# Kernel tuning notes

Measured on AMD Instinct MI355X. Metric: run time of the kernel, lower is better.

## Reference

```python
import jax, jax.numpy as jnp
import numpy as np

B, T, S, D, H, F = 4, 1024, 1024, 1024, 16, 4096
NEG = jnp.float32(-1e9)


def _ln(x, g, b):
    m = jnp.mean(x, axis=-1, keepdims=True)
    v = jnp.mean((x - m) ** 2, axis=-1, keepdims=True)
    return (x - m) * jax.lax.rsqrt(v + 1e-5) * g + b


def _mha(q, k, v, wq, bq, wk, bk, wv, bv, wo, bo, scale, mask, causal, sbias):
    Bq, Tq, Dq = q.shape
    Sk = k.shape[1]
    dk = Dq // H
    Q = (q @ wq.T + bq).reshape(Bq, Tq, H, dk).transpose(0, 2, 1, 3)  # [B,H,T,dk]
    K = (k @ wk.T + bk).reshape(Bq, Sk, H, dk).transpose(0, 2, 1, 3)  # [B,H,S,dk]
    V = (v @ wv.T + bv).reshape(Bq, Sk, H, dk).transpose(0, 2, 1, 3)
    s = jnp.einsum('bhtd,bhsd->bhts', Q, K) / jnp.sqrt(jnp.float32(dk))
    if sbias is not None:
        s = s + scale * sbias[:, None, None, :]
    if mask is not None:
        s = jnp.where(mask == 0, NEG, s)
    if causal is not None:
        s = jnp.where(causal == 0, NEG, s)
    a = jax.nn.softmax(s, axis=-1)
    o = jnp.einsum('bhts,bhsd->bhtd', a, V).transpose(0, 2, 1, 3).reshape(Bq, Tq, Dq)
    return o @ wo.T + bo


def setup_inputs():
    key = jax.random.key(0)
    ks = jax.random.split(key, 16)
    r = lambda i, shape, s=0.02: jax.random.normal(ks[i], shape, dtype=jnp.float32) * s
    z = lambda *shape: jnp.zeros(shape, jnp.float32)
    o = lambda *shape: jnp.ones(shape, jnp.float32)
    inp = dict(
        x=r(0, (B, T, D), 1.0),
        memory=r(1, (B, S, D), 1.0),
        sentence_bias=r(2, (B, S), 1.0),
        trg_mask=jnp.ones((B, 1, 1, T), jnp.int32),
        trg_causal_mask=jnp.tril(jnp.ones((T, T), jnp.int32))[None, None],
        src_mask=jnp.ones((B, 1, 1, S), jnp.int32),
        sa_wq=r(3, (D, D)), sa_bq=z(D), sa_wk=r(4, (D, D)), sa_bk=z(D),
        sa_wv=r(5, (D, D)), sa_bv=z(D), sa_wo=r(6, (D, D)), sa_bo=z(D),
        sa_scale=jnp.float32(0.1),
        ca_wq=r(7, (D, D)), ca_bq=z(D), ca_wk=r(8, (D, D)), ca_bk=z(D),
        ca_wv=r(9, (D, D)), ca_bv=z(D), ca_wo=r(10, (D, D)), ca_bo=z(D),
        ca_scale=jnp.float32(0.1),
        ln1_g=o(D), ln1_b=z(D), ln2_g=o(D), ln2_b=z(D), ln3_g=o(D), ln3_b=z(D),
        ffn_w1=r(11, (F, D)), ffn_b1=z(F), ffn_w2=r(12, (D, F)), ffn_b2=z(D),
    )
    return inp


def reference(x, memory, trg_mask, trg_causal_mask, src_mask, sentence_bias,
              sa_wq, sa_bq, sa_wk, sa_bk, sa_wv, sa_bv, sa_wo, sa_bo, sa_scale,
              ca_wq, ca_bq, ca_wk, ca_bk, ca_wv, ca_bv, ca_wo, ca_bo, ca_scale,
              ln1_g, ln1_b, ln2_g, ln2_b, ln3_g, ln3_b,
              ffn_w1, ffn_b1, ffn_w2, ffn_b2):
    # Faithful quirk: Q comes from normed x, K/V from raw residual stream.
    x = x + _mha(_ln(x, ln1_g, ln1_b), x, x,
                 sa_wq, sa_bq, sa_wk, sa_bk, sa_wv, sa_bv, sa_wo, sa_bo,
                 sa_scale, trg_mask, trg_causal_mask, None)
    x = x + _mha(_ln(x, ln2_g, ln2_b), memory, memory,
                 ca_wq, ca_bq, ca_wk, ca_bk, ca_wv, ca_bv, ca_wo, ca_bo,
                 ca_scale, src_mask, None, sentence_bias)
    h = _ln(x, ln3_g, ln3_b)
    x = x + (jax.nn.relu(h @ ffn_w1.T + ffn_b1) @ ffn_w2.T + ffn_b2)
    return x
```

## Files before the change

### kernel.cpp

```cpp
#include <hip/hip_runtime.h>
#include <hip/hip_bf16.h>
#include <cmath>
#include <stdint.h>

typedef __hip_bfloat16 bf16;
typedef __attribute__((ext_vector_type(8))) __bf16 bf16x8;
typedef __attribute__((ext_vector_type(8))) unsigned short u16x8;
typedef __attribute__((ext_vector_type(4))) float f32x4;

__device__ __forceinline__ void gld16(const void* g, const void* l)
{
    __builtin_amdgcn_global_load_lds(
        (const __attribute__((address_space(1))) unsigned int*)(unsigned long long)g,
        (__attribute__((address_space(3))) unsigned int*)(unsigned int)(unsigned long long)l,
        16, 0, 0);
}

struct CvtSrcs { const float* p[24]; };

__global__ __launch_bounds__(256) void cvt_all(
    CvtSrcs s, bf16* __restrict__ dst,
    const float* __restrict__ lg, const float* __restrict__ lb,
    bf16* __restrict__ lnout)
{
    const int t = threadIdx.x;
    const int i = (blockIdx.x * 256 + t) * 8;
    const int seg = i >> 20;
    const float* sp = s.p[seg] + (i & 1048575);
    const float4 a = *(const float4*)(sp);
    const float4 b = *(const float4*)(sp + 4);
    const float v[8] = {a.x, a.y, a.z, a.w, b.x, b.y, b.z, b.w};
    bf16 tmp[8];
#pragma unroll
    for (int j = 0; j < 8; ++j) tmp[j] = __float2bfloat16(v[j]);
    *(uint4*)(dst + i) = *(const uint4*)tmp;

    if (seg < 4) {
        float s1 = 0.f, s2 = 0.f;
#pragma unroll
        for (int j = 0; j < 8; ++j) { s1 += v[j]; s2 += v[j] * v[j]; }
#pragma unroll
        for (int off = 32; off > 0; off >>= 1) {
            s1 += __shfl_xor(s1, off, 64);
            s2 += __shfl_xor(s2, off, 64);
        }
        __shared__ float r1[4], r2[4];
        const int w = t >> 6;
        if ((t & 63) == 0) { r1[w] = s1; r2[w] = s2; }
        __syncthreads();
        const int rw = (w >> 1) * 2;
        s1 = r1[rw] + r1[rw + 1];
        s2 = r2[rw] + r2[rw + 1];
        const float mean = s1 * (1.f / 1024.f);
        const float var  = s2 * (1.f / 1024.f) - mean * mean;
        const float rstd = rsqrtf(var + 1e-5f);
        bf16 lt[8];
        const int c0 = i & 1023;
#pragma unroll
        for (int j = 0; j < 8; ++j)
            lt[j] = __float2bfloat16((v[j] - mean) * rstd * lg[c0 + j] + lb[c0 + j]);
        *(uint4*)(lnout + i) = *(const uint4*)lt;
    }
}

enum {
    EPI_QSCALE = 0,
    EPI_KV = 1,
    EPI_RELU = 2,
    EPI_RES_F32_F32OUT = 3,
    EPI_PART = 4
};

template <int EPI>
__global__ __launch_bounds__(512, 2) void gemm256(
    const bf16* __restrict__ A, const bf16* __restrict__ W,
    const float* __restrict__ bias, void* __restrict__ out,
    int N, int Kiter, int Kstride)
{
    __shared__ __align__(16) unsigned short sA[2][2][128 * 64];
    __shared__ __align__(16) unsigned short sB[2][2][128 * 64];

    const int t  = threadIdx.x;
    const int l  = t & 63;
    const int w  = t >> 6;
    const int wv = w * 64;
    const int wr = w >> 2;
    const int wc = w & 3;
    const int lm = l & 15;
    const int kq = l >> 4;
    const int rx = lm & 7;

    int bx = blockIdx.x;
    const int xcd = bx & 7;
    const int ib  = bx >> 3;
    const int bm  = xcd * 2 + (ib & 1);
    const int bn  = ib >> 1;

    const bf16* gA = A + (size_t)(bm * 256 + (t >> 3)) * Kstride
                       + ((t & 7) ^ ((t >> 3) & 7)) * 8;
    const bf16* gB = W + (size_t)(bn * 256 + (t >> 3)) * Kstride
                       + ((t & 7) ^ ((t >> 3) & 7)) * 8;

#define SQA(slot, kt, j)                                        \
    gld16(gA + (size_t)((j) * 64) * Kstride + (kt) * 64,        \
          &sA[slot][(j) >> 1][(((j) & 1) * 512 + wv) * 8])
#define SQB(slot, kt, j)                                        \
    gld16(gB + (size_t)((j) * 64) * Kstride + (kt) * 64,        \
          &sB[slot][(j) >> 1][(((j) & 1) * 512 + wv) * 8])

    bf16x8 af[4][2], bg[2][2];

#define READ_AF(s_, mh)                                                     \
    do {                                                                    \
        _Pragma("unroll")                                                   \
        for (int mi = 0; mi < 4; ++mi)                                      \
            _Pragma("unroll")                                               \
            for (int kk = 0; kk < 2; ++kk) {                                \
                const int lr = (mh) * 64 + mi * 16 + lm;                    \
                const int sl = ((kk << 2) | kq) ^ rx;                       \
                af[mi][kk] = __builtin_bit_cast(bf16x8,                     \
                    *(const u16x8*)(&sA[s_][wr][lr * 64 + sl * 8]));        \
            }                                                               \
    } while (0)
#define READ_BG(s_, nh)                                                     \
    do {                                                                    \
        _Pragma("unroll")                                                   \
        for (int ni = 0; ni < 2; ++ni)                                      \
            _Pragma("unroll")                                               \
            for (int kk = 0; kk < 2; ++kk) {                                \
                const int lr = (wc & 1) * 64 + (nh) * 32 + ni * 16 + lm;    \
                const int sl = ((kk << 2) | kq) ^ rx;                       \
                bg[ni][kk] = __builtin_bit_cast(bf16x8,                     \
                    *(const u16x8*)(&sB[s_][wc >> 1][lr * 64 + sl * 8]));   \
            }                                                               \
    } while (0)
#define MFMA_QUAD(mh, nh)                                                   \
    do {                                                                    \
        __builtin_amdgcn_s_setprio(1);                                      \
        _Pragma("unroll")                                                   \
        for (int mi = 0; mi < 4; ++mi)                                      \
            _Pragma("unroll")                                               \
            for (int ni = 0; ni < 2; ++ni)                                  \
                _Pragma("unroll")                                           \
                for (int kk = 0; kk < 2; ++kk)                              \
                    acc[(mh) * 4 + mi][(nh) * 2 + ni] =                     \
                        __builtin_amdgcn_mfma_f32_16x16x32_bf16(            \
                            af[mi][kk], bg[ni][kk],                         \
                            acc[(mh) * 4 + mi][(nh) * 2 + ni], 0, 0, 0);    \
        __builtin_amdgcn_s_setprio(0);                                      \
    } while (0)
#define BARRIER() do { __builtin_amdgcn_s_barrier();                        \
                       __builtin_amdgcn_sched_barrier(0); } while (0)
#define WAITV4() asm volatile("s_waitcnt vmcnt(4)" ::: "memory")
#define WAITV2() asm volatile("s_waitcnt vmcnt(2)" ::: "memory")
#define WAITV0() asm volatile("s_waitcnt vmcnt(0)" ::: "memory")

    f32x4 acc[8][4] = {};
    const int NT = Kiter >> 6;

    SQB(0, 0, 0); SQB(0, 0, 1); SQB(0, 0, 2); SQB(0, 0, 3);
    SQA(0, 0, 0); SQA(0, 0, 2); SQA(0, 0, 1); SQA(0, 0, 3);

    for (int tt = 0; tt < NT - 1; ++tt) {
        const int s = tt & 1, d = s ^ 1, kn = tt + 1;
        WAITV2(); BARRIER();
        SQB(d, kn, 0); SQB(d, kn, 1);
        READ_AF(s, 0); READ_BG(s, 0);
        MFMA_QUAD(0, 0);
        WAITV2(); BARRIER();
        SQB(d, kn, 2); SQB(d, kn, 3);
        READ_AF(s, 1);
        MFMA_QUAD(1, 0);
        SQA(d, kn, 0); SQA(d, kn, 2);
        READ_BG(s, 1);
        MFMA_QUAD(1, 1);
        SQA(d, kn, 1); SQA(d, kn, 3);
        READ_AF(s, 0);
        MFMA_QUAD(0, 1);
    }
    {
        const int s = (NT - 1) & 1;
        WAITV2(); BARRIER();
        READ_AF(s, 0); READ_BG(s, 0);
        MFMA_QUAD(0, 0);
        WAITV0(); BARRIER();
        READ_AF(s, 1);
        MFMA_QUAD(1, 0);
        READ_BG(s, 1);
        MFMA_QUAD(1, 1);
        READ_AF(s, 0);
        MFMA_QUAD(0, 1);
    }

    __syncthreads();
    unsigned short* scr = (w < 4) ? &sA[0][0][0] + w * 8192
                                  : &sB[0][0][0] + (w - 4) * 8192;

#pragma unroll
    for (int NI = 0; NI < 4; ++NI) {
        const int col = bn * 256 + wc * 64 + NI * 16 + lm;
        const float bv = bias[col];
        const int c  = NI * 2 + (lm >> 3);
        const int ci = lm & 7;
#pragma unroll
        for (int MI = 0; MI < 8; ++MI) {
#pragma unroll
            for (int r = 0; r < 4; ++r) {
                float v = acc[MI][NI][r] + bv;
                if (EPI == EPI_RELU) v = fmaxf(v, 0.f);
                const int row = MI * 16 + kq * 4 + r;
                scr[row * 64 + ((c ^ (row & 7)) * 8) + ci] =
                    __builtin_bit_cast(unsigned short, (__bf16)v);
            }
        }
    }
#pragma unroll
    for (int it = 0; it < 16; ++it) {
        const int row = it * 8 + (l >> 3);
        const int lc  = l & 7;
        const u16x8 vv = *(const u16x8*)&scr[row * 64 + ((lc ^ (row & 7)) * 8)];
        const int Crow = bm * 256 + wr * 128 + row;
        const int Ccol = bn * 256 + wc * 64 + lc * 8;
        *(u16x8*)((bf16*)out + (size_t)Crow * N + Ccol) = vv;
    }
#undef SQA
#undef SQB
#undef READ_AF
#undef READ_BG
#undef MFMA_QUAD
}

template <int EPI>
__global__ __launch_bounds__(256, 2) void gemm_bt(
    const bf16* __restrict__ A, const bf16* __restrict__ W,
    const float* __restrict__ bias, const float* __restrict__ bias2,
    const float* __restrict__ res, void* __restrict__ out,
    int M, int N, int Kiter, int Kstride)
{
    __shared__ __align__(16) unsigned short sA[2][128 * 64];
    __shared__ __align__(16) unsigned short sB[2][128 * 64];

    const int t  = threadIdx.x;
    const int l  = t & 63;
    const int w  = t >> 6;
    const int wv = w * 64;
    const int wm = (w >> 1) * 64;
    const int wn = (w & 1) * 64;
    const int lm = l & 15;
    const int kq = l >> 4;
    const int rx = lm & 7;

    const int bx  = blockIdx.x;
    const int xcd = bx & 7;
    const int ib  = bx >> 3;
    const int bm  = xcd * 4 + (ib & 3);
    const int bn  = ib >> 2;

    const bf16* gA = A + (size_t)(bm * 128 + (t >> 3)) * Kstride
                       + ((t & 7) ^ ((t >> 3) & 7)) * 8;
    const bf16* gB = W + (size_t)(bn * 128 + (t >> 3)) * Kstride
                       + ((t & 7) ^ ((t >> 3) & 7)) * 8;

#define SQA(slot, kt, j)                                        \
    gld16(gA + (size_t)((j) * 32) * Kstride + (kt) * 64,        \
          &sA[slot][((j) * 256 + wv) * 8])
#define SQB(slot, kt, j)                                        \
    gld16(gB + (size_t)((j) * 32) * Kstride + (kt) * 64,        \
          &sB[slot][((j) * 256 + wv) * 8])

    bf16x8 af[2][2], bg[2][2];

#define READ_AF(s_, mh)                                                     \
    do {                                                                    \
        _Pragma("unroll")                                                   \
        for (int mi = 0; mi < 2; ++mi)                                      \
            _Pragma("unroll")                                               \
            for (int kk = 0; kk < 2; ++kk) {                                \
                const int lr = wm + (mh) * 32 + mi * 16 + lm;               \
                const int sl = ((kk << 2) | kq) ^ rx;                       \
                af[mi][kk] = __builtin_bit_cast(bf16x8,                     \
                    *(const u16x8*)(&sA[s_][lr * 64 + sl * 8]));            \
            }                                                               \
    } while (0)
#define READ_BG(s_, nh)                                                     \
    do {                                                                    \
        _Pragma("unroll")                                                   \
        for (int ni = 0; ni < 2; ++ni)                                      \
            _Pragma("unroll")                                               \
            for (int kk = 0; kk < 2; ++kk) {                                \
                const int lr = wn + (nh) * 32 + ni * 16 + lm;               \
                const int sl = ((kk << 2) | kq) ^ rx;                       \
                bg[ni][kk] = __builtin_bit_cast(bf16x8,                     \
                    *(const u16x8*)(&sB[s_][lr * 64 + sl * 8]));            \
            }                                                               \
    } while (0)
#define MFMA_QUAD(mh, nh)                                                   \
    do {                                                                    \
        __builtin_amdgcn_s_setprio(1);                                      \
        _Pragma("unroll")                                                   \
        for (int mi = 0; mi < 2; ++mi)                                      \
            _Pragma("unroll")                                               \
            for (int ni = 0; ni < 2; ++ni)                                  \
                _Pragma("unroll")                                           \
                for (int kk = 0; kk < 2; ++kk)                              \
                    acc[(mh) * 2 + mi][(nh) * 2 + ni] =                     \
                        __builtin_amdgcn_mfma_f32_16x16x32_bf16(            \
                            af[mi][kk], bg[ni][kk],                         \
                            acc[(mh) * 2 + mi][(nh) * 2 + ni], 0, 0, 0);    \
        __builtin_amdgcn_s_setprio(0);                                      \
    } while (0)

    f32x4 acc[4][4] = {};
    const int NT = Kiter >> 6;

    SQB(0, 0, 0); SQB(0, 0, 2); SQA(0, 0, 0); SQA(0, 0, 2);
    SQB(0, 0, 1); SQB(0, 0, 3); SQA(0, 0, 1); SQA(0, 0, 3);

    for (int tt = 0; tt < NT - 1; ++tt) {
        const int s = tt & 1, d = s ^ 1, kn = tt + 1;
        WAITV4(); BARRIER();
        SQB(d, kn, 0); SQB(d, kn, 2);
        READ_AF(s, 0); READ_BG(s, 0);
        MFMA_QUAD(0, 0);
        WAITV2(); BARRIER();
        SQA(d, kn, 0); SQA(d, kn, 2);
        READ_AF(s, 1);
        MFMA_QUAD(1, 0);
        SQB(d, kn, 1); SQB(d, kn, 3);
        READ_BG(s, 1);
        MFMA_QUAD(1, 1);
        SQA(d, kn, 1); SQA(d, kn, 3);
        READ_AF(s, 0);
        MFMA_QUAD(0, 1);
    }
    {
        const int s = (NT - 1) & 1;
        WAITV4(); BARRIER();
        READ_AF(s, 0); READ_BG(s, 0);
        MFMA_QUAD(0, 0);
        WAITV0(); BARRIER();
        READ_AF(s, 1);
        MFMA_QUAD(1, 0);
        READ_BG(s, 1);
        MFMA_QUAD(1, 1);
        READ_AF(s, 0);
        MFMA_QUAD(0, 1);
    }
#undef SQA
#undef SQB
#undef READ_AF
#undef READ_BG
#undef MFMA_QUAD
#undef BARRIER
#undef WAITV4
#undef WAITV2
#undef WAITV0

#pragma unroll
    for (int ni = 0; ni < 4; ++ni) {
        const int col = bn * 128 + wn + ni * 16 + lm;
        float bv = 0.f;
        if (EPI == EPI_KV) bv = (col < 1024) ? bias[col] : bias2[col - 1024];
        else bv = bias[col];
#pragma unroll
        for (int mi = 0; mi < 4; ++mi) {
#pragma unroll
            for (int r = 0; r < 4; ++r) {
                const int row = bm * 128 + wm + mi * 16 + kq * 4 + r;
                float v = acc[mi][ni][r] + bv;
                if (EPI == EPI_QSCALE) v *= 0.125f;
                if (EPI == EPI_KV) {
                    if (col < 1024) {
                        ((bf16*)out)[(size_t)row * 1024 + col] = __float2bfloat16(v);
                    } else {
                        const int ch = col - 1024;
                        const size_t idx = (size_t)4 * 1048576 +
                            ((size_t)((row >> 10) * 16 + (ch >> 6)) * 64 + (ch & 63)) * 1024
                            + (row & 1023);
                        ((bf16*)out)[idx] = __float2bfloat16(v);
                    }
                } else if (EPI == EPI_RES_F32_F32OUT) {
                    const size_t idx = (size_t)row * N + col;
                    ((float*)out)[idx] = v + res[idx];
                } else {
                    ((bf16*)out)[(size_t)row * N + col] = __float2bfloat16(v);
                }
            }
        }
    }
}

template <bool CAUSAL, bool SBIAS>
__global__ __launch_bounds__(256, 2) void flash_attn(
    const bf16* __restrict__ Q, const bf16* __restrict__ K,
    const bf16* __restrict__ Vt, bf16* __restrict__ O,
    const float* __restrict__ sbias, const float* __restrict__ scale_ptr)
{
    __shared__ __align__(16) unsigned short sK[2][64 * 64];
    __shared__ __align__(16) unsigned short sV[2][64 * 64];
    __shared__ __align__(16) unsigned short sP[4 * 32 * 72];

    const int t  = threadIdx.x;
    const int l  = t & 63;
    const int w  = t >> 6;
    const int wv = w * 64;
    const int lm = l & 15;
    const int kq = l >> 4;

    const int bh = blockIdx.x & 63;
    const int qb = blockIdx.x >> 6;
    const int h  = bh & 15;
    const int b  = bh >> 4;

    const int tb = qb * 128 + w * 32;
    const size_t qrow0 = (size_t)(b * 1024 + tb) * 1024 + h * 64;

    bf16x8 qf[2][2];
#pragma unroll
    for (int mi = 0; mi < 2; ++mi)
#pragma unroll
        for (int kk = 0; kk < 2; ++kk)
            qf[mi][kk] = __builtin_bit_cast(bf16x8,
                *(const u16x8*)(Q + qrow0 + (size_t)(mi * 16 + lm) * 1024 + kk * 32 + kq * 8));

    float cs = 0.f; const float* sb = nullptr;
    if (SBIAS) { cs = scale_ptr[0]; sb = sbias + b * 1024; }

    const bf16* gK = K  + (size_t)(b * 1024 + (t >> 3)) * 1024 + h * 64
                   + ((t & 7) ^ ((t >> 3) & 7)) * 8;
    const bf16* gV = Vt + (size_t)((b * 16 + h) * 64 + (t >> 3)) * 1024
                   + ((t & 7) ^ ((t >> 3) & 7)) * 8;
    __bf16* sPw = (__bf16*)sP + w * 32 * 72;

#define STAGE_KV(buf, s0r)                                                   \
    do {                                                                     \
        gld16(gK + (size_t)(s0r) * 1024,        &sK[buf][wv * 8]);           \
        gld16(gK + (size_t)((s0r) + 32) * 1024, &sK[buf][2048 + wv * 8]);    \
        gld16(gV + (s0r),                       &sV[buf][wv * 8]);           \
        gld16(gV + (s0r) + 32 * 1024,           &sV[buf][2048 + wv * 8]);    \
    } while (0)

    const int niter = CAUSAL ? (2 * qb + 2) : 16;

    STAGE_KV(0, 0);
    __syncthreads();

    f32x4 acc_o[2][4] = {};
    f32x4 l_run[2] = {};

    for (int it = 0; it < niter; ++it) {
        const int s0 = it * 64;
        const int cur = it & 1;

        if (it + 1 < niter) STAGE_KV(cur ^ 1, s0 + 64);

        f32x4 accs[2][4] = {};
#pragma unroll
        for (int ni = 0; ni < 4; ++ni)
#pragma unroll
            for (int kk = 0; kk < 2; ++kk) {
                const bf16x8 kf = __builtin_bit_cast(bf16x8,
                    *(const u16x8*)(&sK[cur][(ni * 16 + lm) * 64
                        + ((((kk << 2) | kq)) ^ (lm & 7)) * 8]));
#pragma unroll
                for (int mi = 0; mi < 2; ++mi)
                    accs[mi][ni] = __builtin_amdgcn_mfma_f32_16x16x32_bf16(
                        qf[mi][kk], kf, accs[mi][ni], 0, 0, 0);
            }

        if (SBIAS) {
#pragma unroll
            for (int ni = 0; ni < 4; ++ni) {
                const float sv = cs * sb[s0 + ni * 16 + lm];
#pragma unroll
                for (int mi = 0; mi < 2; ++mi)
#pragma unroll
                    for (int r = 0; r < 4; ++r) accs[mi][ni][r] += sv;
            }
        }
        if (CAUSAL && (s0 + 63 > tb)) {
#pragma unroll
            for (int ni = 0; ni < 4; ++ni) {
                const int s = s0 + ni * 16 + lm;
#pragma unroll
                for (int mi = 0; mi < 2; ++mi)
#pragma unroll
                    for (int r = 0; r < 4; ++r)
                        if (s > tb + mi * 16 + kq * 4 + r) accs[mi][ni][r] = -1e30f;
            }
        }

#pragma unroll
        for (int mi = 0; mi < 2; ++mi)
#pragma unroll
            for (int ni = 0; ni < 4; ++ni)
#pragma unroll
                for (int r = 0; r < 4; ++r) {
                    const float e = __expf(accs[mi][ni][r]);
                    l_run[mi][r] += e;
                    sPw[(mi * 16 + kq * 4 + r) * 72 + ni * 16 + lm] = (__bf16)e;
                }

#pragma unroll
        for (int kk = 0; kk < 2; ++kk) {
            bf16x8 pf[2];
#pragma unroll
            for (int mi = 0; mi < 2; ++mi)
                pf[mi] = __builtin_bit_cast(bf16x8,
                    *(const u16x8*)(sPw + (mi * 16 + lm) * 72 + kk * 32 + kq * 8));
#pragma unroll
            for (int di = 0; di < 4; ++di) {
                const bf16x8 vf = __builtin_bit_cast(bf16x8,
                    *(const u16x8*)(&sV[cur][(di * 16 + lm) * 64
                        + ((((kk << 2) | kq)) ^ (lm & 7)) * 8]));
#pragma unroll
                for (int mi = 0; mi < 2; ++mi)
                    acc_o[mi][di] = __builtin_amdgcn_mfma_f32_16x16x32_bf16(
                        pf[mi], vf, acc_o[mi][di], 0, 0, 0);
            }
        }

        __syncthreads();
    }
#undef STAGE_KV

#pragma unroll
    for (int mi = 0; mi < 2; ++mi) {
        f32x4 lt = l_run[mi];
#pragma unroll
        for (int x = 1; x < 16; x <<= 1)
#pragma unroll
            for (int r = 0; r < 4; ++r) lt[r] += __shfl_xor(lt[r], x, 64);
#pragma unroll
        for (int r = 0; r < 4; ++r) lt[r] = 1.f / lt[r];
#pragma unroll
        for (int di = 0; di < 4; ++di)
#pragma unroll
            for (int r = 0; r < 4; ++r) {
                const size_t idx = (size_t)(b * 1024 + tb + mi * 16 + kq * 4 + r) * 1024
                                 + h * 64 + di * 16 + lm;
                O[idx] = __float2bfloat16(acc_o[mi][di][r] * lt[r]);
            }
    }
}

__global__ __launch_bounds__(256) void ln_kernel(
    const float* __restrict__ xin, const float* __restrict__ g,
    const float* __restrict__ bta, bf16* __restrict__ out)
{
    const int row = blockIdx.x;
    const int t = threadIdx.x;
    const size_t base = (size_t)row * 1024 + t * 4;

    const float4 f = *(const float4*)(xin + base);
    const float v[4] = {f.x, f.y, f.z, f.w};
    float s1 = v[0] + v[1] + v[2] + v[3];
    float s2 = v[0]*v[0] + v[1]*v[1] + v[2]*v[2] + v[3]*v[3];
#pragma unroll
    for (int off = 32; off > 0; off >>= 1) {
        s1 += __shfl_xor(s1, off, 64);
        s2 += __shfl_xor(s2, off, 64);
    }
    __shared__ float r1[4], r2[4];
    if ((t & 63) == 0) { r1[t >> 6] = s1; r2[t >> 6] = s2; }
    __syncthreads();
    s1 = r1[0] + r1[1] + r1[2] + r1[3];
    s2 = r2[0] + r2[1] + r2[2] + r2[3];
    const float mean = s1 * (1.f / 1024.f);
    const float var  = s2 * (1.f / 1024.f) - mean * mean;
    const float rstd = rsqrtf(var + 1e-5f);
#pragma unroll
    for (int j = 0; j < 4; ++j) {
        const int c = t * 4 + j;
        out[base + j] = __float2bfloat16((v[j] - mean) * rstd * g[c] + bta[c]);
    }
}

extern "C" void kernel_launch(void* const* d_in, const int* in_sizes, int n_in,
                              void* d_out, int out_size, void* d_ws, size_t ws_size,
                              hipStream_t stream)
{
    const float* x       = (const float*)d_in[0];
    const float* memory  = (const float*)d_in[1];
    const float* sbias   = (const float*)d_in[2];
    const float* sa_bq = (const float*)d_in[7];
    const float* sa_bk = (const float*)d_in[9];
    const float* sa_bv = (const float*)d_in[11];
    const float* sa_bo = (const float*)d_in[13];
    const float* ca_bq = (const float*)d_in[16];
    const float* ca_bk = (const float*)d_in[18];
    const float* ca_bv = (const float*)d_in[20];
    const float* ca_bo = (const float*)d_in[22];
    const float* ca_scale = (const float*)d_in[23];
    const float* ln1_g = (const float*)d_in[24]; const float* ln1_b = (const float*)d_in[25];
    const float* ln2_g = (const float*)d_in[26]; const float* ln2_b = (const float*)d_in[27];
    const float* ln3_g = (const float*)d_in[28]; const float* ln3_b = (const float*)d_in[29];
    const float* b1 = (const float*)d_in[31];
    const float* b2 = (const float*)d_in[33];

    char* ws = (char*)d_ws;
    const size_t MB = (size_t)1 << 20;
    float* x1    = (float*)(ws + 0 * MB);
    float* x2    = (float*)(ws + 16 * MB);
    bf16* lnbuf  = (bf16*)(ws + 32 * MB);
    bf16* Qb     = (bf16*)(ws + 40 * MB);
    bf16* Kb     = (bf16*)(ws + 48 * MB);
    bf16* Vtb    = (bf16*)(ws + 56 * MB);
    bf16* Ob     = (bf16*)(ws + 64 * MB);
    bf16* ffnmid = (bf16*)(ws + 40 * MB);
    bf16* wx     = (bf16*)(ws + 72 * MB);
    bf16* wmem   = (bf16*)(ws + 80 * MB);
    bf16* bw     = (bf16*)(ws + 88 * MB);
    bf16* b_sa_wq = bw + 0 * 1048576, *b_sa_wk = bw + 1 * 1048576;
    bf16* b_sa_wo = bw + 3 * 1048576;
    bf16* b_ca_wq = bw + 4 * 1048576, *b_ca_wk = bw + 5 * 1048576;
    bf16* b_ca_wo = bw + 7 * 1048576;
    bf16* b_w1   = (bf16*)(ws + 104 * MB);
    bf16* b_w2   = (bf16*)(ws + 112 * MB);

    const int M = 4096;
    dim3 blk256(256), blk512(512);
    const dim3 gQ(256);
    const dim3 gKV(512);
    const dim3 gFA(512);
    const dim3 g256(256);

    CvtSrcs cs;
    for (int c = 0; c < 4; ++c) {
        cs.p[c]      = x + (size_t)c * 1048576;
        cs.p[4 + c]  = memory + (size_t)c * 1048576;
        cs.p[16 + c] = (const float*)d_in[30] + (size_t)c * 1048576;
        cs.p[20 + c] = (const float*)d_in[32] + (size_t)c * 1048576;
    }
    cs.p[8]  = (const float*)d_in[6];
    cs.p[9]  = (const float*)d_in[8];
    cs.p[10] = (const float*)d_in[10];
    cs.p[11] = (const float*)d_in[12];
    cs.p[12] = (const float*)d_in[15];
    cs.p[13] = (const float*)d_in[17];
    cs.p[14] = (const float*)d_in[19];
    cs.p[15] = (const float*)d_in[21];
    cvt_all<<<24 * 1048576 / 2048, blk256, 0, stream>>>(
        cs, wx, ln1_g, ln1_b, lnbuf);

    gemm_bt<EPI_QSCALE><<<gQ, blk256, 0, stream>>>(
        lnbuf, b_sa_wq, sa_bq, nullptr, nullptr, Qb, M, 1024, 1024, 1024);
    gemm_bt<EPI_KV><<<gKV, blk256, 0, stream>>>(
        wx, b_sa_wk, sa_bk, sa_bv, nullptr, Kb, M, 2048, 1024, 1024);
    flash_attn<true, false><<<gFA, blk256, 0, stream>>>(Qb, Kb, Vtb, Ob, nullptr, nullptr);
    gemm_bt<EPI_RES_F32_F32OUT><<<gQ, blk256, 0, stream>>>(
        Ob, b_sa_wo, sa_bo, nullptr, x, x1, M, 1024, 1024, 1024);

    ln_kernel<<<4096, blk256, 0, stream>>>(x1, ln2_g, ln2_b, lnbuf);
    gemm_bt<EPI_QSCALE><<<gQ, blk256, 0, stream>>>(
        lnbuf, b_ca_wq, ca_bq, nullptr, nullptr, Qb, M, 1024, 1024, 1024);
    gemm_bt<EPI_KV><<<gKV, blk256, 0, stream>>>(
        wmem, b_ca_wk, ca_bk, ca_bv, nullptr, Kb, M, 2048, 1024, 1024);
    flash_attn<false, true><<<gFA, blk256, 0, stream>>>(Qb, Kb, Vtb, Ob, sbias, ca_scale);
    gemm_bt<EPI_RES_F32_F32OUT><<<gQ, blk256, 0, stream>>>(
        Ob, b_ca_wo, ca_bo, nullptr, x1, x2, M, 1024, 1024, 1024);

    ln_kernel<<<4096, blk256, 0, stream>>>(x2, ln3_g, ln3_b, lnbuf);
    gemm256<EPI_RELU><<<g256, blk512, 0, stream>>>(
        lnbuf, b_w1, b1, ffnmid, 4096, 1024, 1024);
    gemm_bt<EPI_RES_F32_F32OUT><<<gQ, blk256, 0, stream>>>(
        ffnmid, b_w2, b2, nullptr, x2, d_out, M, 1024, 4096, 4096);
}
```

Before: 457.6 us.

## Shrink gemm_bt N-tile to 64 and double grid for Q/KV projections

Changes the generic bf16 GEMM tile from 128x128 to 128x64, so each wave computes a 64x32 sub-tile and the B shared buffer is halved. The K-loop schedule is rewritten around per-k-half phases, and the launch bound is raised to allow three blocks per CU. The Q and KV projection grids double to cover the narrower tiles. The goal is more blocks and better occupancy on the small 1024-wide projections, at the cost of lower operand reuse per tile and more A reloads.

```diff
diff --git a/kernel.cpp b/kernel.cpp
--- a/kernel.cpp
+++ b/kernel.cpp
@@ -151,7 +151,6 @@
     } while (0)
 #define BARRIER() do { __builtin_amdgcn_s_barrier();                        \
                        __builtin_amdgcn_sched_barrier(0); } while (0)
-#define WAITV4() asm volatile("s_waitcnt vmcnt(4)" ::: "memory")
 #define WAITV2() asm volatile("s_waitcnt vmcnt(2)" ::: "memory")
 #define WAITV0() asm volatile("s_waitcnt vmcnt(0)" ::: "memory")
 
@@ -231,21 +230,21 @@
 }
 
 template <int EPI>
-__global__ __launch_bounds__(256, 2) void gemm_bt(
+__global__ __launch_bounds__(256, 3) void gemm_bt(
     const bf16* __restrict__ A, const bf16* __restrict__ W,
     const float* __restrict__ bias, const float* __restrict__ bias2,
     const float* __restrict__ res, void* __restrict__ out,
     int M, int N, int Kiter, int Kstride)
 {
     __shared__ __align__(16) unsigned short sA[2][128 * 64];
-    __shared__ __align__(16) unsigned short sB[2][128 * 64];
+    __shared__ __align__(16) unsigned short sB[2][64 * 64];
 
     const int t  = threadIdx.x;
     const int l  = t & 63;
     const int w  = t >> 6;
     const int wv = w * 64;
-    const int wm = (w >> 1) * 64;
-    const int wn = (w & 1) * 64;
+    const int wr = w >> 1;
+    const int wc = w & 1;
     const int lm = l & 15;
     const int kq = l >> 4;
     const int rx = lm & 7;
@@ -258,7 +257,7 @@
 
     const bf16* gA = A + (size_t)(bm * 128 + (t >> 3)) * Kstride
                        + ((t & 7) ^ ((t >> 3) & 7)) * 8;
-    const bf16* gB = W + (size_t)(bn * 128 + (t >> 3)) * Kstride
+    const bf16* gB = W + (size_t)(bn * 64 + (t >> 3)) * Kstride
                        + ((t & 7) ^ ((t >> 3) & 7)) * 8;
 
 #define SQA(slot, kt, j)                                        \
@@ -268,97 +267,95 @@
     gld16(gB + (size_t)((j) * 32) * Kstride + (kt) * 64,        \
           &sB[slot][((j) * 256 + wv) * 8])
 
-    bf16x8 af[2][2], bg[2][2];
-
-#define READ_AF(s_, mh)                                                     \
+    bf16x8 af[4][2], bg[2][2];
+
+#define READ_A(s_, mh, kk)                                                  \
     do {                                                                    \
         _Pragma("unroll")                                                   \
-        for (int mi = 0; mi < 2; ++mi)                                      \
-            _Pragma("unroll")                                               \
-            for (int kk = 0; kk < 2; ++kk) {                                \
-                const int lr = wm + (mh) * 32 + mi * 16 + lm;               \
-                const int sl = ((kk << 2) | kq) ^ rx;                       \
-                af[mi][kk] = __builtin_bit_cast(bf16x8,                     \
-                    *(const u16x8*)(&sA[s_][lr * 64 + sl * 8]));            \
-            }                                                               \
+        for (int m2 = 0; m2 < 2; ++m2) {                                    \
+            const int mi = (mh) * 2 + m2;                                   \
+            const int lr = wr * 64 + mi * 16 + lm;                          \
+            const int sl = (((kk) << 2) | kq) ^ rx;                         \
+            af[mi][kk] = __builtin_bit_cast(bf16x8,                         \
+                *(const u16x8*)(&sA[s_][lr * 64 + sl * 8]));                \
+        }                                                                   \
     } while (0)
-#define READ_BG(s_, nh)                                                     \
+#define READ_B(s_, kk)                                                      \
     do {                                                                    \
         _Pragma("unroll")                                                   \
-        for (int ni = 0; ni < 2; ++ni)                                      \
-            _Pragma("unroll")                                               \
-            for (int kk = 0; kk < 2; ++kk) {                                \
-                const int lr = wn + (nh) * 32 + ni * 16 + lm;               \
-                const int sl = ((kk << 2) | kq) ^ rx;                       \
-                bg[ni][kk] = __builtin_bit_cast(bf16x8,                     \
-                    *(const u16x8*)(&sB[s_][lr * 64 + sl * 8]));            \
-            }                                                               \
+        for (int ni = 0; ni < 2; ++ni) {                                    \
+            const int lr = wc * 32 + ni * 16 + lm;                          \
+            const int sl = (((kk) << 2) | kq) ^ rx;                         \
+            bg[ni][kk] = __builtin_bit_cast(bf16x8,                         \
+                *(const u16x8*)(&sB[s_][lr * 64 + sl * 8]));                \
+        }                                                                   \
     } while (0)
-#define MFMA_QUAD(mh, nh)                                                   \
+#define MFMA_PH(mh, kk)                                                     \
     do {                                                                    \
         __builtin_amdgcn_s_setprio(1);                                      \
         _Pragma("unroll")                                                   \
-        for (int mi = 0; mi < 2; ++mi)                                      \
+        for (int m2 = 0; m2 < 2; ++m2)                                      \
             _Pragma("unroll")                                               \
             for (int ni = 0; ni < 2; ++ni)                                  \
-                _Pragma("unroll")                                           \
-                for (int kk = 0; kk < 2; ++kk)                              \
-                    acc[(mh) * 2 + mi][(nh) * 2 + ni] =                     \
-                        __builtin_amdgcn_mfma_f32_16x16x32_bf16(            \
-                            af[mi][kk], bg[ni][kk],                         \
-                            acc[(mh) * 2 + mi][(nh) * 2 + ni], 0, 0, 0);    \
+                acc[(mh) * 2 + m2][ni] =                                    \
+                    __builtin_amdgcn_mfma_f32_16x16x32_bf16(                \
+                        af[(mh) * 2 + m2][kk], bg[ni][kk],                  \
+                        acc[(mh) * 2 + m2][ni], 0, 0, 0);                   \
         __builtin_amdgcn_s_setprio(0);                                      \
     } while (0)
-
-    f32x4 acc[4][4] = {};
+#define BARRIER() do { __builtin_amdgcn_s_barrier();                        \
+                       __builtin_amdgcn_sched_barrier(0); } while (0)
+#define WAITV2() asm volatile("s_waitcnt vmcnt(2)" ::: "memory")
+#define WAITV0() asm volatile("s_waitcnt vmcnt(0)" ::: "memory")
+
+    f32x4 acc[4][2] = {};
     const int NT = Kiter >> 6;
 
-    SQB(0, 0, 0); SQB(0, 0, 2); SQA(0, 0, 0); SQA(0, 0, 2);
-    SQB(0, 0, 1); SQB(0, 0, 3); SQA(0, 0, 1); SQA(0, 0, 3);
+    SQB(0, 0, 0); SQB(0, 0, 1);
+    SQA(0, 0, 0); SQA(0, 0, 2);
+    SQA(0, 0, 1); SQA(0, 0, 3);
 
     for (int tt = 0; tt < NT - 1; ++tt) {
         const int s = tt & 1, d = s ^ 1, kn = tt + 1;
-        WAITV4(); BARRIER();
-        SQB(d, kn, 0); SQB(d, kn, 2);
-        READ_AF(s, 0); READ_BG(s, 0);
-        MFMA_QUAD(0, 0);
+        WAITV2(); BARRIER();
+        SQB(d, kn, 0); SQB(d, kn, 1);
+        READ_A(s, 0, 0); READ_B(s, 0);
+        MFMA_PH(0, 0);
         WAITV2(); BARRIER();
         SQA(d, kn, 0); SQA(d, kn, 2);
-        READ_AF(s, 1);
-        MFMA_QUAD(1, 0);
-        SQB(d, kn, 1); SQB(d, kn, 3);
-        READ_BG(s, 1);
-        MFMA_QUAD(1, 1);
+        READ_A(s, 1, 0);
+        MFMA_PH(1, 0);
         SQA(d, kn, 1); SQA(d, kn, 3);
-        READ_AF(s, 0);
-        MFMA_QUAD(0, 1);
+        READ_A(s, 1, 1); READ_B(s, 1);
+        MFMA_PH(1, 1);
+        READ_A(s, 0, 1);
+        MFMA_PH(0, 1);
     }
     {
         const int s = (NT - 1) & 1;
-        WAITV4(); BARRIER();
-        READ_AF(s, 0); READ_BG(s, 0);
-        MFMA_QUAD(0, 0);
+        WAITV2(); BARRIER();
+        READ_A(s, 0, 0); READ_B(s, 0);
+        MFMA_PH(0, 0);
         WAITV0(); BARRIER();
-        READ_AF(s, 1);
-        MFMA_QUAD(1, 0);
-        READ_BG(s, 1);
-        MFMA_QUAD(1, 1);
-        READ_AF(s, 0);
-        MFMA_QUAD(0, 1);
+        READ_A(s, 1, 0);
+        MFMA_PH(1, 0);
+        READ_A(s, 1, 1); READ_B(s, 1);
+        MFMA_PH(1, 1);
+        READ_A(s, 0, 1);
+        MFMA_PH(0, 1);
     }
 #undef SQA
 #undef SQB
-#undef READ_AF
-#undef READ_BG
-#undef MFMA_QUAD
+#undef READ_A
+#undef READ_B
+#undef MFMA_PH
 #undef BARRIER
-#undef WAITV4
 #undef WAITV2
 #undef WAITV0
 
 #pragma unroll
-    for (int ni = 0; ni < 4; ++ni) {
-        const int col = bn * 128 + wn + ni * 16 + lm;
+    for (int ni = 0; ni < 2; ++ni) {
+        const int col = bn * 64 + wc * 32 + ni * 16 + lm;
         float bv = 0.f;
         if (EPI == EPI_KV) bv = (col < 1024) ? bias[col] : bias2[col - 1024];
         else bv = bias[col];
@@ -366,7 +363,7 @@
         for (int mi = 0; mi < 4; ++mi) {
 #pragma unroll
             for (int r = 0; r < 4; ++r) {
-                const int row = bm * 128 + wm + mi * 16 + kq * 4 + r;
+                const int row = bm * 128 + wr * 64 + mi * 16 + kq * 4 + r;
                 float v = acc[mi][ni][r] + bv;
                 if (EPI == EPI_QSCALE) v *= 0.125f;
                 if (EPI == EPI_KV) {
@@ -620,8 +617,8 @@
 
     const int M = 4096;
     dim3 blk256(256), blk512(512);
-    const dim3 gQ(256);
-    const dim3 gKV(512);
+    const dim3 gQ(512);
+    const dim3 gKV(1024);
     const dim3 gFA(512);
     const dim3 g256(256);
 
```

Result: no change. 457.3 us (-0.1%).
